# Kernel optimization log

Measured on AMD Instinct MI355X. Metric: run time of the kernel, lower is better.

The kernel has to match this reference:

```python
import jax, jax.numpy as jnp
import numpy as np

N_HEAD = 16
N_FEAT = 1024
D_K = N_FEAT // N_HEAD


def setup_inputs() -> dict:
    key = jax.random.key(0)
    ks = jax.random.split(key, 11)
    B, T1, T2 = 2, 2048, 2048
    s = 0.02
    return {
        "query": jax.random.normal(ks[0], (B, T1, N_FEAT), jnp.float32),
        "key_": jax.random.normal(ks[1], (B, T2, N_FEAT), jnp.float32),
        "value": jax.random.normal(ks[2], (B, T2, N_FEAT), jnp.float32),
        "mask": jnp.ones((B, T1, T2), jnp.int32),
        "Wq": jax.random.normal(ks[3], (N_FEAT, N_FEAT), jnp.float32) * s,
        "bq": jnp.zeros((N_FEAT,), jnp.float32),
        "Wk": jax.random.normal(ks[4], (N_FEAT, N_FEAT), jnp.float32) * s,
        "bk": jnp.zeros((N_FEAT,), jnp.float32),
        "Wv": jax.random.normal(ks[5], (N_FEAT, N_FEAT), jnp.float32) * s,
        "bv": jnp.zeros((N_FEAT,), jnp.float32),
        "Wo": jax.random.normal(ks[6], (N_FEAT, N_FEAT), jnp.float32) * s,
        "bo": jnp.zeros((N_FEAT,), jnp.float32),
    }


def reference(query, key_, value, mask, Wq, bq, Wk, bk, Wv, bv, Wo, bo):
    B = query.shape[0]
    # project and split heads: (B, T, F) -> (B, H, T, d_k)
    def heads(x, W, b):
        y = x @ W + b
        return y.reshape(B, -1, N_HEAD, D_K).transpose(0, 2, 1, 3)

    q = heads(query, Wq, bq)
    k = heads(key_, Wk, bk)
    v = heads(value, Wv, bv)

    scale = jnp.sqrt(jnp.asarray(D_K, jnp.float32))
    scores = jnp.einsum("bhqd,bhkd->bhqk", q, k) / scale  # (B,H,T1,T2)
    m = mask[:, None, :, :]  # (B,1,T1,T2)
    scores = jnp.where(m > 0, scores, jnp.asarray(-10000.0, scores.dtype))
    attn = jax.nn.softmax(scores, axis=-1)
    # dropout_rate = 0.0 / inference -> identity
    x = jnp.einsum("bhqk,bhkd->bhqd", attn, v)
    x = x.transpose(0, 2, 1, 3).reshape(B, -1, N_FEAT)
    return x @ Wo + bo
```

## Files before the change

kernel.cpp:

```cpp
#include <hip/hip_runtime.h>
#include <hip/hip_bf16.h>
#include <stdint.h>

typedef float  f32x4 __attribute__((ext_vector_type(4)));
typedef short  s16x8 __attribute__((ext_vector_type(8)));
typedef short  s16x4 __attribute__((ext_vector_type(4)));
typedef int    i32x4 __attribute__((ext_vector_type(4)));

#define DI __device__ __forceinline__

constexpr int Bb = 2, Tt = 2048, Ff = 1024, Hh = 16, Dk = 64;
constexpr int Mm = Bb * Tt;
constexpr float LOG2E = 1.44269504088896340736f;

DI ushort f2bf(float f) {
  unsigned u = __float_as_uint(f);
  unsigned r = (u + 0x7fffu + ((u >> 16) & 1u)) >> 16;
  return (ushort)r;
}

DI int cvt_pk_bf16(float lo, float hi) {
  __hip_bfloat162 t = __float22bfloat162_rn(make_float2(lo, hi));
  int w;
  __builtin_memcpy(&w, &t, 4);
  return w;
}

DI void gload16(const void* g, void* l) {
  __builtin_amdgcn_global_load_lds(
      (__attribute__((address_space(1))) void*)g,
      (__attribute__((address_space(3))) void*)l, 16, 0, 0);
}

DI void wait_vm4() { asm volatile("s_waitcnt vmcnt(4)" ::: "memory"); }
DI void wait_vm0() { asm volatile("s_waitcnt vmcnt(0)" ::: "memory"); }

__global__ __launch_bounds__(256) void prep_kernel(
    const float* __restrict__ s0, const float* __restrict__ s1, const float* __restrict__ s2,
    ushort* __restrict__ d0, ushort* __restrict__ d1, ushort* __restrict__ d2,
    const float* __restrict__ W0, const float* __restrict__ W1,
    const float* __restrict__ W2, const float* __restrict__ W3,
    ushort* __restrict__ Wt0, ushort* __restrict__ Wt1,
    ushort* __restrict__ Wt2, ushort* __restrict__ Wt3,
    const int* __restrict__ mask, int* __restrict__ flags) {
  const int bid = blockIdx.x;
  const int t = threadIdx.x;
  if (bid < 6144) {
    const int z = bid >> 11, x = bid & 2047;
    const float* src = z == 0 ? s0 : (z == 1 ? s1 : s2);
    ushort* dst = z == 0 ? d0 : (z == 1 ? d1 : d2);
    const int i = x * 256 + t;
    const float4* s4 = (const float4*)src + (size_t)i * 2;
    float4 a = s4[0], b = s4[1];
    s16x8 o;
    o[0] = (short)f2bf(a.x); o[1] = (short)f2bf(a.y); o[2] = (short)f2bf(a.z); o[3] = (short)f2bf(a.w);
    o[4] = (short)f2bf(b.x); o[5] = (short)f2bf(b.y); o[6] = (short)f2bf(b.z); o[7] = (short)f2bf(b.w);
    *((s16x8*)dst + i) = o;
  } else if (bid < 7168) {
    const int wb = bid - 6144;
    const int z = wb >> 8, bx = wb & 15, by = (wb >> 4) & 15;
    const float* W; ushort* Wt;
    switch (z) {
      case 0: W = W0; Wt = Wt0; break;
      case 1: W = W1; Wt = Wt1; break;
      case 2: W = W2; Wt = Wt2; break;
      default: W = W3; Wt = Wt3; break;
    }
    __shared__ float tile[64][65];
    const int k0 = by * 64, n0 = bx * 64;
    const int r = t >> 4, c4 = (t & 15) * 4;
#pragma unroll
    for (int i = 0; i < 4; i++) {
      const int row = r + i * 16;
      const float4 v = *(const float4*)(W + (size_t)(k0 + row) * Ff + n0 + c4);
      tile[row][c4] = v.x; tile[row][c4 + 1] = v.y; tile[row][c4 + 2] = v.z; tile[row][c4 + 3] = v.w;
    }
    __syncthreads();
#pragma unroll
    for (int i = 0; i < 4; i++) {
      const int n = r + i * 16;
      s16x4 o;
#pragma unroll
      for (int j = 0; j < 4; j++) o[j] = (short)f2bf(tile[c4 + j][n]);
      *(s16x4*)(Wt + (size_t)(n0 + n) * Ff + k0 + c4) = o;
    }
  } else {
    const int mb = bid - 7168;
    const int kb = mb & 31, qb = (mb >> 5) & 31, bz = mb >> 10;
    __shared__ int s;
    if (t == 0) s = 1;
    __syncthreads();
    int ok = 1;
#pragma unroll
    for (int i = 0; i < 4; i++) {
      const int row = qb * 64 + (t >> 4) + i * 16;
      const int4 v = *(const int4*)(mask + ((size_t)bz * Tt + row) * Tt + kb * 64 + (t & 15) * 4);
      ok &= (v.x > 0) & (v.y > 0) & (v.z > 0) & (v.w > 0);
    }
    atomicAnd(&s, ok);
    __syncthreads();
    if (t == 0) flags[(bz * 32 + qb) * 32 + kb] = s;
  }
}

DI void gemm_core(const ushort* __restrict__ A, const ushort* __restrict__ Bt,
                  const float* __restrict__ bias, void* __restrict__ Cout, float scale, int mode,
                  int m0, int n0) {
  __shared__ ushort Ads[3][128 * 32];
  __shared__ ushort Bds[3][128 * 32];
  const int tid = threadIdx.x, lane = tid & 63, w = tid >> 6;
  const int wr = w >> 1, wc = w & 1;
  const int g = lane >> 4, ln = lane & 15;
  const int strow = tid >> 2;
  const int stc = (tid & 3) * 8;

  const ushort* Asrc0 = A + (size_t)(m0 + strow) * Ff + stc;
  const ushort* Asrc1 = A + (size_t)(m0 + 64 + strow) * Ff + stc;
  const ushort* Bsrc0 = Bt + (size_t)(n0 + strow) * Ff + stc;
  const ushort* Bsrc1 = Bt + (size_t)(n0 + 64 + strow) * Ff + stc;
  const int dst0 = strow * 32 + stc;
  const int dst1 = (64 + strow) * 32 + stc;

  f32x4 acc[4][4];
#pragma unroll
  for (int m = 0; m < 4; m++)
#pragma unroll
    for (int n = 0; n < 4; n++) acc[m][n] = (f32x4){0.f, 0.f, 0.f, 0.f};

  auto stage = [&](int t, int slot) {
    const int k0 = t * 32;
    gload16(Asrc0 + k0, Ads[slot] + dst0);
    gload16(Asrc1 + k0, Ads[slot] + dst1);
    gload16(Bsrc0 + k0, Bds[slot] + dst0);
    gload16(Bsrc1 + k0, Bds[slot] + dst1);
  };

  stage(0, 0);
  stage(1, 1);

  int rs = 0, ws = 2;
  for (int t = 0; t < 32; ++t) {
    if (t < 31) wait_vm4(); else wait_vm0();
    __builtin_amdgcn_s_barrier();
    __builtin_amdgcn_sched_barrier(0);
    if (t < 30) stage(t + 2, ws);
    const ushort* As = Ads[rs];
    const ushort* Bs = Bds[rs];
    s16x8 af[4], bf[4];
#pragma unroll
    for (int m = 0; m < 4; m++) af[m] = *(const s16x8*)(As + (wr * 64 + m * 16 + ln) * 32 + g * 8);
#pragma unroll
    for (int n = 0; n < 4; n++) bf[n] = *(const s16x8*)(Bs + (wc * 64 + n * 16 + ln) * 32 + g * 8);
    __builtin_amdgcn_s_setprio(1);
#pragma unroll
    for (int m = 0; m < 4; m++)
#pragma unroll
      for (int n = 0; n < 4; n++)
        acc[m][n] = __builtin_amdgcn_mfma_f32_16x16x32_bf16(af[m], bf[n], acc[m][n], 0, 0, 0);
    __builtin_amdgcn_s_setprio(0);
    rs = rs == 2 ? 0 : rs + 1;
    ws = ws == 2 ? 0 : ws + 1;
  }
#pragma unroll
  for (int m = 0; m < 4; m++) {
    const int r0 = m0 + wr * 64 + m * 16 + g * 4;
#pragma unroll
    for (int n = 0; n < 4; n++) {
      const int col = n0 + wc * 64 + n * 16 + ln;
      const float bv = bias[col];
      if (mode == 2) {
        const int bb = r0 >> 11, rb = r0 & 2047;
        const int x = rb & 63;
        const int pbase = (x & 0x20) | ((x & 0x0C) << 1) | ((x & 0x10) >> 2);
        s16x4 o4;
#pragma unroll
        for (int r = 0; r < 4; r++) o4[r] = (short)f2bf(acc[m][n][r] + bv);
        *(s16x4*)((ushort*)Cout + ((size_t)bb * Ff + col) * Tt + (rb & ~63) + pbase) = o4;
      } else {
#pragma unroll
        for (int r = 0; r < 4; r++) {
          const float val = (acc[m][n][r] + bv) * scale;
          if (mode == 1)
            ((ushort*)Cout)[(size_t)(r0 + r) * Ff + col] = f2bf(val);
          else
            ((float*)Cout)[(size_t)(r0 + r) * Ff + col] = val;
        }
      }
    }
  }
}

__global__ __launch_bounds__(256) void qkv_gemm_kernel(
    const ushort* __restrict__ Xq, const ushort* __restrict__ Xk, const ushort* __restrict__ Xv,
    const ushort* __restrict__ Wqt, const ushort* __restrict__ Wkt, const ushort* __restrict__ Wvt,
    const float* __restrict__ bq, const float* __restrict__ bk, const float* __restrict__ bv,
    ushort* __restrict__ Qb, ushort* __restrict__ Kb, ushort* __restrict__ Vpt) {
  const int lin = blockIdx.x + 8 * blockIdx.y + 256 * blockIdx.z;
  const int work = (lin & 7) * 96 + (lin >> 3);
  const int z = work >> 8;
  const int r = work & 255;
  const int m0 = (r >> 3) * 128, n0 = (r & 7) * 128;
  const ushort* A = z == 0 ? Xq : (z == 1 ? Xk : Xv);
  const ushort* Wt = z == 0 ? Wqt : (z == 1 ? Wkt : Wvt);
  const float* bias = z == 0 ? bq : (z == 1 ? bk : bv);
  void* C = z == 0 ? (void*)Qb : (z == 1 ? (void*)Kb : (void*)Vpt);
  const float scale = z == 0 ? 0.125f * LOG2E : 1.0f;
  gemm_core(A, Wt, bias, C, scale, z == 2 ? 2 : 1, m0, n0);
}

__global__ __launch_bounds__(256) void out_gemm_kernel(const ushort* __restrict__ AO,
                                                       const ushort* __restrict__ Wot,
                                                       const float* __restrict__ bo,
                                                       float* __restrict__ Out) {
  const int lin = blockIdx.x + 8 * blockIdx.y;
  const int work = (lin & 7) * 32 + (lin >> 3);
  const int m0 = (work >> 3) * 128, n0 = (work & 7) * 128;
  gemm_core(AO, Wot, bo, Out, 1.0f, 0, m0, n0);
}

__global__ __launch_bounds__(256) void flash_kernel(
    const ushort* __restrict__ Qb, const ushort* __restrict__ Kb, const ushort* __restrict__ Vpt,
    const int* __restrict__ flags, const int* __restrict__ mask, ushort* __restrict__ AO) {
  __shared__ ushort Ks[4][64 * 64];
  __shared__ ushort Vs[4][64 * 64];
  const int lin = blockIdx.x + 16 * (blockIdx.y + 16 * blockIdx.z);
  const int work = (lin & 7) * 64 + (lin >> 3);
  const int qb = work & 15, h = (work >> 4) & 15, b = work >> 8;
  const int tid = threadIdx.x, lane = tid & 63, w = tid >> 6;
  const int g = lane >> 4, ln = lane & 15;

  const ushort* Qg = Qb + ((size_t)b * Tt + qb * 128) * Ff + h * Dk;
  const ushort* Kg = Kb + ((size_t)b * Tt) * Ff + h * Dk;
  const ushort* Vg = Vpt + (size_t)(b * Ff + h * Dk) * Tt;

  const int srow = lane >> 3;
  const int swzch = ((lane & 7) ^ srow) * 8;

  const ushort* ksrc0 = Kg + (size_t)(w * 16 + srow) * Ff + swzch;
  const ushort* ksrc1 = ksrc0 + (size_t)8 * Ff;
  const ushort* vsrc0 = Vg + (size_t)(w * 16 + srow) * Tt + swzch;
  const ushort* vsrc1 = vsrc0 + (size_t)8 * Tt;

  s16x8 qf0[2], qf1[2];
  {
    const ushort* Qrow0 = Qg + (size_t)(w * 16 + ln) * Ff;
    const ushort* Qrow1 = Qrow0 + (size_t)64 * Ff;
    qf0[0] = *(const s16x8*)(Qrow0 + g * 8);
    qf0[1] = *(const s16x8*)(Qrow0 + 32 + g * 8);
    qf1[0] = *(const s16x8*)(Qrow1 + g * 8);
    qf1[1] = *(const s16x8*)(Qrow1 + 32 + g * 8);
  }
  const int* flagrow0 = flags + (b * 32 + qb * 2) * 32;
  const int f0 = (lane < 32) ? flagrow0[lane] : 1;
  const int f1 = (lane < 32) ? flagrow0[32 + lane] : 1;

  auto stage2 = [&](ushort* Kd0, ushort* Vd0, ushort* Kd1, ushort* Vd1) {
    const int r0 = w * 16;
    gload16(ksrc0, Kd0 + r0 * 64);
    gload16(ksrc1, Kd0 + (r0 + 8) * 64);
    gload16(vsrc0, Vd0 + r0 * 64);
    gload16(vsrc1, Vd0 + (r0 + 8) * 64);
    gload16(ksrc0 + (size_t)64 * Ff, Kd1 + r0 * 64);
    gload16(ksrc1 + (size_t)64 * Ff, Kd1 + (r0 + 8) * 64);
    gload16(vsrc0 + 64, Vd1 + r0 * 64);
    gload16(vsrc1 + 64, Vd1 + (r0 + 8) * 64);
    ksrc0 += (size_t)128 * Ff; ksrc1 += (size_t)128 * Ff;
    vsrc0 += 128; vsrc1 += 128;
  };

  stage2(Ks[0], Vs[0], Ks[1], Vs[1]);
  stage2(Ks[2], Vs[2], Ks[3], Vs[3]);
  __syncthreads();
  const unsigned long long bm0 = __ballot(f0 == 0);
  const unsigned long long bm1 = __ballot(f1 == 0);

  int loff[4][2];
#pragma unroll
  for (int i = 0; i < 4; i++)
#pragma unroll
    for (int c = 0; c < 2; c++) {
      const int row = i * 16 + ln;
      loff[i][c] = row * 128 + ((c * 64 + g * 16) ^ ((row & 7) << 4));
    }
  const char* Kbase = (const char*)&Ks[0][0];
  const char* Vbase = (const char*)&Vs[0][0];

  s16x8 onesf;
#pragma unroll
  for (int j = 0; j < 8; ++j) onesf[j] = (short)0x3F80;

  f32x4 accl0 = (f32x4){0.f, 0.f, 0.f, 0.f}, accl1 = (f32x4){0.f, 0.f, 0.f, 0.f};
  f32x4 o0[4], o1[4];
#pragma unroll
  for (int ds = 0; ds < 4; ds++) { o0[ds] = (f32x4){0.f, 0.f, 0.f, 0.f}; o1[ds] = (f32x4){0.f, 0.f, 0.f, 0.f}; }

  auto body = [&](int slot, int kt) {
    const char* Kc = Kbase + slot * 8192;
    const char* Vc = Vbase + slot * 8192;
    f32x4 sf0[4], sf1[4];
    __builtin_amdgcn_s_setprio(1);
#pragma unroll
    for (int ks = 0; ks < 4; ++ks) {
      f32x4 a0 = (f32x4){0.f, 0.f, 0.f, 0.f};
      f32x4 a1 = (f32x4){0.f, 0.f, 0.f, 0.f};
#pragma unroll
      for (int c = 0; c < 2; c++) {
        const s16x8 kf = *(const s16x8*)(Kc + loff[ks][c]);
        a0 = __builtin_amdgcn_mfma_f32_16x16x32_bf16(kf, qf0[c], a0, 0, 0, 0);
        a1 = __builtin_amdgcn_mfma_f32_16x16x32_bf16(kf, qf1[c], a1, 0, 0, 0);
      }
      sf0[ks] = a0; sf1[ks] = a1;
    }
    __builtin_amdgcn_s_setprio(0);
    if ((bm0 >> kt) & 1ull) {
      const int qg_ = qb * 128 + w * 16 + ln;
#pragma unroll
      for (int ks = 0; ks < 4; ++ks) {
        const int4 mv = *(const int4*)(mask + ((size_t)b * Tt + qg_) * Tt + kt * 64 + ks * 16 + g * 4);
        if (mv.x <= 0) sf0[ks][0] = -10000.f;
        if (mv.y <= 0) sf0[ks][1] = -10000.f;
        if (mv.z <= 0) sf0[ks][2] = -10000.f;
        if (mv.w <= 0) sf0[ks][3] = -10000.f;
      }
    }
    if ((bm1 >> kt) & 1ull) {
      const int qg_ = qb * 128 + 64 + w * 16 + ln;
#pragma unroll
      for (int ks = 0; ks < 4; ++ks) {
        const int4 mv = *(const int4*)(mask + ((size_t)b * Tt + qg_) * Tt + kt * 64 + ks * 16 + g * 4);
        if (mv.x <= 0) sf1[ks][0] = -10000.f;
        if (mv.y <= 0) sf1[ks][1] = -10000.f;
        if (mv.z <= 0) sf1[ks][2] = -10000.f;
        if (mv.w <= 0) sf1[ks][3] = -10000.f;
      }
    }
#pragma unroll
    for (int ks = 0; ks < 4; ++ks) {
#pragma unroll
      for (int r = 0; r < 4; ++r) {
        sf0[ks][r] = __builtin_amdgcn_exp2f(sf0[ks][r]);
        sf1[ks][r] = __builtin_amdgcn_exp2f(sf1[ks][r]);
      }
    }
    i32x4 paw0[2], paw1[2];
#pragma unroll
    for (int c = 0; c < 2; c++)
#pragma unroll
      for (int f = 0; f < 2; f++)
#pragma unroll
        for (int hh = 0; hh < 2; hh++) {
          paw0[c][f * 2 + hh] = cvt_pk_bf16(sf0[2 * c + f][2 * hh], sf0[2 * c + f][2 * hh + 1]);
          paw1[c][f * 2 + hh] = cvt_pk_bf16(sf1[2 * c + f][2 * hh], sf1[2 * c + f][2 * hh + 1]);
        }
    const s16x8 pa00 = __builtin_bit_cast(s16x8, paw0[0]);
    const s16x8 pa01 = __builtin_bit_cast(s16x8, paw0[1]);
    const s16x8 pa10 = __builtin_bit_cast(s16x8, paw1[0]);
    const s16x8 pa11 = __builtin_bit_cast(s16x8, paw1[1]);
    __builtin_amdgcn_s_setprio(1);
    accl0 = __builtin_amdgcn_mfma_f32_16x16x32_bf16(pa00, onesf, accl0, 0, 0, 0);
    accl0 = __builtin_amdgcn_mfma_f32_16x16x32_bf16(pa01, onesf, accl0, 0, 0, 0);
    accl1 = __builtin_amdgcn_mfma_f32_16x16x32_bf16(pa10, onesf, accl1, 0, 0, 0);
    accl1 = __builtin_amdgcn_mfma_f32_16x16x32_bf16(pa11, onesf, accl1, 0, 0, 0);
#pragma unroll
    for (int ds = 0; ds < 4; ++ds) {
#pragma unroll
      for (int c = 0; c < 2; ++c) {
        const s16x8 vf = *(const s16x8*)(Vc + loff[ds][c]);
        o0[ds] = __builtin_amdgcn_mfma_f32_16x16x32_bf16(c == 0 ? pa00 : pa01, vf, o0[ds], 0, 0, 0);
        o1[ds] = __builtin_amdgcn_mfma_f32_16x16x32_bf16(c == 0 ? pa10 : pa11, vf, o1[ds], 0, 0, 0);
      }
    }
    __builtin_amdgcn_s_setprio(0);
  };

  for (int kt = 0; kt < 32; kt += 4) {
    body(0, kt);
    body(1, kt + 1);
    __syncthreads();
    if (kt + 4 < 32) stage2(Ks[0], Vs[0], Ks[1], Vs[1]);
    body(2, kt + 2);
    body(3, kt + 3);
    __syncthreads();
    if (kt + 6 < 32) stage2(Ks[2], Vs[2], Ks[3], Vs[3]);
  }

  float inv0[4], inv1[4];
#pragma unroll
  for (int r = 0; r < 4; ++r) {
    inv0[r] = 1.0f / accl0[r];
    inv1[r] = 1.0f / accl1[r];
  }
  ushort* AOg0 = AO + ((size_t)b * Tt + qb * 128 + w * 16) * Ff + h * Dk;
  ushort* AOg1 = AOg0 + (size_t)64 * Ff;
#pragma unroll
  for (int ds = 0; ds < 4; ++ds)
#pragma unroll
    for (int r = 0; r < 4; ++r) {
      AOg0[(size_t)(g * 4 + r) * Ff + ds * 16 + ln] = f2bf(o0[ds][r] * inv0[r]);
      AOg1[(size_t)(g * 4 + r) * Ff + ds * 16 + ln] = f2bf(o1[ds][r] * inv1[r]);
    }
}

extern "C" void kernel_launch(void* const* d_in, const int* in_sizes, int n_in,
                              void* d_out, int out_size, void* d_ws, size_t ws_size,
                              hipStream_t stream) {
  const float* query = (const float*)d_in[0];
  const float* key_  = (const float*)d_in[1];
  const float* value = (const float*)d_in[2];
  const int*   mask  = (const int*)d_in[3];
  const float* Wq = (const float*)d_in[4];  const float* bq = (const float*)d_in[5];
  const float* Wk = (const float*)d_in[6];  const float* bk = (const float*)d_in[7];
  const float* Wv = (const float*)d_in[8];  const float* bv = (const float*)d_in[9];
  const float* Wo = (const float*)d_in[10]; const float* bo = (const float*)d_in[11];
  float* Out = (float*)d_out;

  constexpr size_t SZ_X = (size_t)Mm * Ff * 2;
  constexpr size_t SZ_W = (size_t)Ff * Ff * 2;
  uintptr_t p = (uintptr_t)d_ws;
  auto alloc = [&](size_t sz) { void* r = (void*)p; p += (sz + 255) & ~(size_t)255; return r; };
  ushort* Xq = (ushort*)alloc(SZ_X);
  ushort* Xk = (ushort*)alloc(SZ_X);
  ushort* Xv = (ushort*)alloc(SZ_X);
  ushort* Wqt = (ushort*)alloc(SZ_W);
  ushort* Wkt = (ushort*)alloc(SZ_W);
  ushort* Wvt = (ushort*)alloc(SZ_W);
  ushort* Wot = (ushort*)alloc(SZ_W);
  ushort* Qp  = (ushort*)alloc(SZ_X);
  ushort* Kp  = (ushort*)alloc(SZ_X);
  ushort* Vpt = (ushort*)alloc(SZ_X);
  int* flags = (int*)alloc((size_t)Bb * 32 * 32 * 4);
  ushort* AO = Xq;

  prep_kernel<<<dim3(9216), 256, 0, stream>>>(query, key_, value, Xq, Xk, Xv,
                                              Wq, Wk, Wv, Wo, Wqt, Wkt, Wvt, Wot,
                                              mask, flags);
  qkv_gemm_kernel<<<dim3(8, 32, 3), 256, 0, stream>>>(Xq, Xk, Xv, Wqt, Wkt, Wvt, bq, bk, bv, Qp, Kp, Vpt);
  flash_kernel<<<dim3(16, 16, 2), 256, 0, stream>>>(Qp, Kp, Vpt, flags, mask, AO);
  out_gemm_kernel<<<dim3(8, 32), 256, 0, stream>>>(AO, Wot, bo, Out);
}
```

Measured before the change: 132.6 us.

## Software-pipeline QK of next tile with softmax/PV of current tile

Restructures the attention main loop so the QK^T MFMAs for tile k+1 are issued before the mask/exp/PV work of tile k, using two ping-pong score register sets. K/V staging changes from paired double-buffer loads to single-tile loads into a 4-slot ring, with a barrier after every tile and one tile prefetched three steps ahead. The aim is to overlap MFMA work with the exp/convert VALU work and to smooth global-to-LDS loads. In exchange it adds more register pressure from the extra score arrays, twice as many barriers, and drops the setprio hints around the QK MFMAs.

Result: slower. 150.3 us (+13.3%).

```diff
diff --git a/kernel.cpp b/kernel.cpp
--- a/kernel.cpp
+++ b/kernel.cpp
@@ -254,22 +254,19 @@
   const int f0 = (lane < 32) ? flagrow0[lane] : 1;
   const int f1 = (lane < 32) ? flagrow0[32 + lane] : 1;
 
-  auto stage2 = [&](ushort* Kd0, ushort* Vd0, ushort* Kd1, ushort* Vd1) {
+  auto stage1 = [&](ushort* Kd, ushort* Vd) {
     const int r0 = w * 16;
-    gload16(ksrc0, Kd0 + r0 * 64);
-    gload16(ksrc1, Kd0 + (r0 + 8) * 64);
-    gload16(vsrc0, Vd0 + r0 * 64);
-    gload16(vsrc1, Vd0 + (r0 + 8) * 64);
-    gload16(ksrc0 + (size_t)64 * Ff, Kd1 + r0 * 64);
-    gload16(ksrc1 + (size_t)64 * Ff, Kd1 + (r0 + 8) * 64);
-    gload16(vsrc0 + 64, Vd1 + r0 * 64);
-    gload16(vsrc1 + 64, Vd1 + (r0 + 8) * 64);
-    ksrc0 += (size_t)128 * Ff; ksrc1 += (size_t)128 * Ff;
-    vsrc0 += 128; vsrc1 += 128;
+    gload16(ksrc0, Kd + r0 * 64);
+    gload16(ksrc1, Kd + (r0 + 8) * 64);
+    gload16(vsrc0, Vd + r0 * 64);
+    gload16(vsrc1, Vd + (r0 + 8) * 64);
+    ksrc0 += (size_t)64 * Ff; ksrc1 += (size_t)64 * Ff;
+    vsrc0 += 64; vsrc1 += 64;
   };
 
-  stage2(Ks[0], Vs[0], Ks[1], Vs[1]);
-  stage2(Ks[2], Vs[2], Ks[3], Vs[3]);
+  stage1(Ks[0], Vs[0]);
+  stage1(Ks[1], Vs[1]);
+  stage1(Ks[2], Vs[2]);
   __syncthreads();
   const unsigned long long bm0 = __ballot(f0 == 0);
   const unsigned long long bm1 = __ballot(f1 == 0);
@@ -288,60 +285,57 @@
   s16x8 onesf;
 #pragma unroll
   for (int j = 0; j < 8; ++j) onesf[j] = (short)0x3F80;
-
-  f32x4 accl0 = (f32x4){0.f, 0.f, 0.f, 0.f}, accl1 = (f32x4){0.f, 0.f, 0.f, 0.f};
+  const f32x4 zz = (f32x4){0.f, 0.f, 0.f, 0.f};
+
+  f32x4 accl0 = zz, accl1 = zz;
   f32x4 o0[4], o1[4];
 #pragma unroll
-  for (int ds = 0; ds < 4; ds++) { o0[ds] = (f32x4){0.f, 0.f, 0.f, 0.f}; o1[ds] = (f32x4){0.f, 0.f, 0.f, 0.f}; }
-
-  auto body = [&](int slot, int kt) {
-    const char* Kc = Kbase + slot * 8192;
-    const char* Vc = Vbase + slot * 8192;
-    f32x4 sf0[4], sf1[4];
-    __builtin_amdgcn_s_setprio(1);
+  for (int ds = 0; ds < 4; ds++) { o0[ds] = zz; o1[ds] = zz; }
+
+  auto qk = [&](const char* Kc, f32x4 (&s0)[4], f32x4 (&s1)[4]) {
 #pragma unroll
     for (int ks = 0; ks < 4; ++ks) {
-      f32x4 a0 = (f32x4){0.f, 0.f, 0.f, 0.f};
-      f32x4 a1 = (f32x4){0.f, 0.f, 0.f, 0.f};
-#pragma unroll
-      for (int c = 0; c < 2; c++) {
-        const s16x8 kf = *(const s16x8*)(Kc + loff[ks][c]);
-        a0 = __builtin_amdgcn_mfma_f32_16x16x32_bf16(kf, qf0[c], a0, 0, 0, 0);
-        a1 = __builtin_amdgcn_mfma_f32_16x16x32_bf16(kf, qf1[c], a1, 0, 0, 0);
+      const s16x8 kfa = *(const s16x8*)(Kc + loff[ks][0]);
+      const s16x8 kfb = *(const s16x8*)(Kc + loff[ks][1]);
+      f32x4 a0 = __builtin_amdgcn_mfma_f32_16x16x32_bf16(kfa, qf0[0], zz, 0, 0, 0);
+      a0 = __builtin_amdgcn_mfma_f32_16x16x32_bf16(kfb, qf0[1], a0, 0, 0, 0);
+      f32x4 a1 = __builtin_amdgcn_mfma_f32_16x16x32_bf16(kfa, qf1[0], zz, 0, 0, 0);
+      a1 = __builtin_amdgcn_mfma_f32_16x16x32_bf16(kfb, qf1[1], a1, 0, 0, 0);
+      s0[ks] = a0; s1[ks] = a1;
+    }
+  };
+
+  auto finish = [&](int ktv, f32x4 (&s0)[4], f32x4 (&s1)[4], const char* Vc) {
+    if ((bm0 >> ktv) & 1ull) {
+      const int qg_ = qb * 128 + w * 16 + ln;
+#pragma unroll
+      for (int ks = 0; ks < 4; ++ks) {
+        const int4 mv = *(const int4*)(mask + ((size_t)b * Tt + qg_) * Tt + ktv * 64 + ks * 16 + g * 4);
+        if (mv.x <= 0) s0[ks][0] = -10000.f;
+        if (mv.y <= 0) s0[ks][1] = -10000.f;
+        if (mv.z <= 0) s0[ks][2] = -10000.f;
+        if (mv.w <= 0) s0[ks][3] = -10000.f;
       }
-      sf0[ks] = a0; sf1[ks] = a1;
-    }
-    __builtin_amdgcn_s_setprio(0);
-    if ((bm0 >> kt) & 1ull) {
-      const int qg_ = qb * 128 + w * 16 + ln;
+    }
+    if ((bm1 >> ktv) & 1ull) {
+      const int qg_ = qb * 128 + 64 + w * 16 + ln;
 #pragma unroll
       for (int ks = 0; ks < 4; ++ks) {
-        const int4 mv = *(const int4*)(mask + ((size_t)b * Tt + qg_) * Tt + kt * 64 + ks * 16 + g * 4);
-        if (mv.x <= 0) sf0[ks][0] = -10000.f;
-        if (mv.y <= 0) sf0[ks][1] = -10000.f;
-        if (mv.z <= 0) sf0[ks][2] = -10000.f;
-        if (mv.w <= 0) sf0[ks][3] = -10000.f;
+        const int4 mv = *(const int4*)(mask + ((size_t)b * Tt + qg_) * Tt + ktv * 64 + ks * 16 + g * 4);
+        if (mv.x <= 0) s1[ks][0] = -10000.f;
+        if (mv.y <= 0) s1[ks][1] = -10000.f;
+        if (mv.z <= 0) s1[ks][2] = -10000.f;
+        if (mv.w <= 0) s1[ks][3] = -10000.f;
       }
     }
-    if ((bm1 >> kt) & 1ull) {
-      const int qg_ = qb * 128 + 64 + w * 16 + ln;
-#pragma unroll
-      for (int ks = 0; ks < 4; ++ks) {
-        const int4 mv = *(const int4*)(mask + ((size_t)b * Tt + qg_) * Tt + kt * 64 + ks * 16 + g * 4);
-        if (mv.x <= 0) sf1[ks][0] = -10000.f;
-        if (mv.y <= 0) sf1[ks][1] = -10000.f;
-        if (mv.z <= 0) sf1[ks][2] = -10000.f;
-        if (mv.w <= 0) sf1[ks][3] = -10000.f;
+#pragma unroll
+    for (int ks = 0; ks < 4; ++ks) {
+#pragma unroll
+      for (int r = 0; r < 4; ++r) {
+        s0[ks][r] = __builtin_amdgcn_exp2f(s0[ks][r]);
+        s1[ks][r] = __builtin_amdgcn_exp2f(s1[ks][r]);
       }
     }
-#pragma unroll
-    for (int ks = 0; ks < 4; ++ks) {
-#pragma unroll
-      for (int r = 0; r < 4; ++r) {
-        sf0[ks][r] = __builtin_amdgcn_exp2f(sf0[ks][r]);
-        sf1[ks][r] = __builtin_amdgcn_exp2f(sf1[ks][r]);
-      }
-    }
     i32x4 paw0[2], paw1[2];
 #pragma unroll
     for (int c = 0; c < 2; c++)
@@ -349,8 +343,8 @@
       for (int f = 0; f < 2; f++)
 #pragma unroll
         for (int hh = 0; hh < 2; hh++) {
-          paw0[c][f * 2 + hh] = cvt_pk_bf16(sf0[2 * c + f][2 * hh], sf0[2 * c + f][2 * hh + 1]);
-          paw1[c][f * 2 + hh] = cvt_pk_bf16(sf1[2 * c + f][2 * hh], sf1[2 * c + f][2 * hh + 1]);
+          paw0[c][f * 2 + hh] = cvt_pk_bf16(s0[2 * c + f][2 * hh], s0[2 * c + f][2 * hh + 1]);
+          paw1[c][f * 2 + hh] = cvt_pk_bf16(s1[2 * c + f][2 * hh], s1[2 * c + f][2 * hh + 1]);
         }
     const s16x8 pa00 = __builtin_bit_cast(s16x8, paw0[0]);
     const s16x8 pa01 = __builtin_bit_cast(s16x8, paw0[1]);
@@ -373,15 +367,26 @@
     __builtin_amdgcn_s_setprio(0);
   };
 
+  f32x4 sA0[4], sA1[4], sB0[4], sB1[4];
+  qk(Kbase, sA0, sA1);
+
   for (int kt = 0; kt < 32; kt += 4) {
-    body(0, kt);
-    body(1, kt + 1);
-    __syncthreads();
-    if (kt + 4 < 32) stage2(Ks[0], Vs[0], Ks[1], Vs[1]);
-    body(2, kt + 2);
-    body(3, kt + 3);
-    __syncthreads();
-    if (kt + 6 < 32) stage2(Ks[2], Vs[2], Ks[3], Vs[3]);
+    qk(Kbase + 8192, sB0, sB1);
+    finish(kt, sA0, sA1, Vbase);
+    __syncthreads();
+    if (kt + 3 < 32) stage1(Ks[3], Vs[3]);
+    qk(Kbase + 2 * 8192, sA0, sA1);
+    finish(kt + 1, sB0, sB1, Vbase + 8192);
+    __syncthreads();
+    if (kt + 4 < 32) stage1(Ks[0], Vs[0]);
+    qk(Kbase + 3 * 8192, sB0, sB1);
+    finish(kt + 2, sA0, sA1, Vbase + 2 * 8192);
+    __syncthreads();
+    if (kt + 5 < 32) stage1(Ks[1], Vs[1]);
+    if (kt + 4 < 32) qk(Kbase, sA0, sA1);
+    finish(kt + 3, sB0, sB1, Vbase + 3 * 8192);
+    __syncthreads();
+    if (kt + 6 < 32) stage1(Ks[2], Vs[2]);
   }
 
   float inv0[4], inv1[4];
```

## Fuse fp32-to-bf16 activation conversion into QKV GEMM loads

Applied to the files above, without the earlier changes.

Removes the separate conversion pass that wrote bf16 copies of query/key/value, and instead has the QKV GEMM load fp32 activation tiles into registers, pack them to bf16, and write them to LDS with a register-staged triple-buffer pipeline. This eliminates a full read/write pass over the activations and reduces workspace. In exchange the GEMM reads twice the bytes for A tiles (repeated across column blocks) and uses more registers and VALU packing work in the main loop.

Result: faster. 124.8 us (-5.9%).

```diff
diff --git a/kernel.cpp b/kernel.cpp
--- a/kernel.cpp
+++ b/kernel.cpp
@@ -26,6 +26,13 @@
   return w;
 }
 
+DI s16x8 pack8(const float4& a, const float4& b) {
+  i32x4 w;
+  w[0] = cvt_pk_bf16(a.x, a.y); w[1] = cvt_pk_bf16(a.z, a.w);
+  w[2] = cvt_pk_bf16(b.x, b.y); w[3] = cvt_pk_bf16(b.z, b.w);
+  return __builtin_bit_cast(s16x8, w);
+}
+
 DI void gload16(const void* g, void* l) {
   __builtin_amdgcn_global_load_lds(
       (__attribute__((address_space(1))) void*)g,
@@ -33,11 +40,11 @@
 }
 
 DI void wait_vm4() { asm volatile("s_waitcnt vmcnt(4)" ::: "memory"); }
+DI void wait_vm6() { asm volatile("s_waitcnt vmcnt(6)" ::: "memory"); }
 DI void wait_vm0() { asm volatile("s_waitcnt vmcnt(0)" ::: "memory"); }
+DI void wait_lgkm0() { asm volatile("s_waitcnt lgkmcnt(0)" ::: "memory"); }
 
 __global__ __launch_bounds__(256) void prep_kernel(
-    const float* __restrict__ s0, const float* __restrict__ s1, const float* __restrict__ s2,
-    ushort* __restrict__ d0, ushort* __restrict__ d1, ushort* __restrict__ d2,
     const float* __restrict__ W0, const float* __restrict__ W1,
     const float* __restrict__ W2, const float* __restrict__ W3,
     ushort* __restrict__ Wt0, ushort* __restrict__ Wt1,
@@ -45,20 +52,8 @@
     const int* __restrict__ mask, int* __restrict__ flags) {
   const int bid = blockIdx.x;
   const int t = threadIdx.x;
-  if (bid < 6144) {
-    const int z = bid >> 11, x = bid & 2047;
-    const float* src = z == 0 ? s0 : (z == 1 ? s1 : s2);
-    ushort* dst = z == 0 ? d0 : (z == 1 ? d1 : d2);
-    const int i = x * 256 + t;
-    const float4* s4 = (const float4*)src + (size_t)i * 2;
-    float4 a = s4[0], b = s4[1];
-    s16x8 o;
-    o[0] = (short)f2bf(a.x); o[1] = (short)f2bf(a.y); o[2] = (short)f2bf(a.z); o[3] = (short)f2bf(a.w);
-    o[4] = (short)f2bf(b.x); o[5] = (short)f2bf(b.y); o[6] = (short)f2bf(b.z); o[7] = (short)f2bf(b.w);
-    *((s16x8*)dst + i) = o;
-  } else if (bid < 7168) {
-    const int wb = bid - 6144;
-    const int z = wb >> 8, bx = wb & 15, by = (wb >> 4) & 15;
+  if (bid < 1024) {
+    const int z = bid >> 8, bx = bid & 15, by = (bid >> 4) & 15;
     const float* W; ushort* Wt;
     switch (z) {
       case 0: W = W0; Wt = Wt0; break;
@@ -85,7 +80,7 @@
       *(s16x4*)(Wt + (size_t)(n0 + n) * Ff + k0 + c4) = o;
     }
   } else {
-    const int mb = bid - 7168;
+    const int mb = bid - 1024;
     const int kb = mb & 31, qb = (mb >> 5) & 31, bz = mb >> 10;
     __shared__ int s;
     if (t == 0) s = 1;
@@ -168,6 +163,98 @@
     for (int n = 0; n < 4; n++) {
       const int col = n0 + wc * 64 + n * 16 + ln;
       const float bv = bias[col];
+#pragma unroll
+      for (int r = 0; r < 4; r++) {
+        const float val = (acc[m][n][r] + bv) * scale;
+        if (mode == 1)
+          ((ushort*)Cout)[(size_t)(r0 + r) * Ff + col] = f2bf(val);
+        else
+          ((float*)Cout)[(size_t)(r0 + r) * Ff + col] = val;
+      }
+    }
+  }
+}
+
+DI void gemm_core_f32a(const float* __restrict__ A, const ushort* __restrict__ Bt,
+                       const float* __restrict__ bias, void* __restrict__ Cout, float scale,
+                       int mode, int m0, int n0) {
+  __shared__ ushort Ads[3][128 * 32];
+  __shared__ ushort Bds[3][128 * 32];
+  const int tid = threadIdx.x, lane = tid & 63, w = tid >> 6;
+  const int wr = w >> 1, wc = w & 1;
+  const int g = lane >> 4, ln = lane & 15;
+  const int strow = tid >> 2;
+  const int stc = (tid & 3) * 8;
+
+  const float*  Asrc0 = A + (size_t)(m0 + strow) * Ff + stc;
+  const float*  Asrc1 = A + (size_t)(m0 + 64 + strow) * Ff + stc;
+  const ushort* Bsrc0 = Bt + (size_t)(n0 + strow) * Ff + stc;
+  const ushort* Bsrc1 = Bt + (size_t)(n0 + 64 + strow) * Ff + stc;
+  const int dst0 = strow * 32 + stc;
+  const int dst1 = (64 + strow) * 32 + stc;
+
+  float4 rA0a, rA0b, rA1a, rA1b;
+  auto loadA = [&](int t) {
+    const float* p0 = Asrc0 + t * 32;
+    const float* p1 = Asrc1 + t * 32;
+    rA0a = *(const float4*)p0; rA0b = *(const float4*)(p0 + 4);
+    rA1a = *(const float4*)p1; rA1b = *(const float4*)(p1 + 4);
+  };
+  auto writeA = [&](int slot) {
+    *(s16x8*)(Ads[slot] + dst0) = pack8(rA0a, rA0b);
+    *(s16x8*)(Ads[slot] + dst1) = pack8(rA1a, rA1b);
+  };
+  auto stageB = [&](int t, int slot) {
+    const int k0 = t * 32;
+    gload16(Bsrc0 + k0, Bds[slot] + dst0);
+    gload16(Bsrc1 + k0, Bds[slot] + dst1);
+  };
+
+  f32x4 acc[4][4];
+#pragma unroll
+  for (int m = 0; m < 4; m++)
+#pragma unroll
+    for (int n = 0; n < 4; n++) acc[m][n] = (f32x4){0.f, 0.f, 0.f, 0.f};
+
+  loadA(0);
+  writeA(0);
+  stageB(0, 0);
+  loadA(1);
+  stageB(1, 1);
+
+  int rs = 0, ps = 1, ws = 2;
+  for (int t = 0; t < 32; ++t) {
+    if (t < 31) wait_vm6(); else wait_vm0();
+    wait_lgkm0();
+    __builtin_amdgcn_s_barrier();
+    __builtin_amdgcn_sched_barrier(0);
+    if (t < 31) writeA(ps);
+    if (t < 30) { loadA(t + 2); stageB(t + 2, ws); }
+    const ushort* As = Ads[rs];
+    const ushort* Bs = Bds[rs];
+    s16x8 af[4], bf[4];
+#pragma unroll
+    for (int m = 0; m < 4; m++) af[m] = *(const s16x8*)(As + (wr * 64 + m * 16 + ln) * 32 + g * 8);
+#pragma unroll
+    for (int n = 0; n < 4; n++) bf[n] = *(const s16x8*)(Bs + (wc * 64 + n * 16 + ln) * 32 + g * 8);
+    __builtin_amdgcn_s_setprio(1);
+#pragma unroll
+    for (int m = 0; m < 4; m++)
+#pragma unroll
+      for (int n = 0; n < 4; n++)
+        acc[m][n] = __builtin_amdgcn_mfma_f32_16x16x32_bf16(af[m], bf[n], acc[m][n], 0, 0, 0);
+    __builtin_amdgcn_s_setprio(0);
+    rs = rs == 2 ? 0 : rs + 1;
+    ps = ps == 2 ? 0 : ps + 1;
+    ws = ws == 2 ? 0 : ws + 1;
+  }
+#pragma unroll
+  for (int m = 0; m < 4; m++) {
+    const int r0 = m0 + wr * 64 + m * 16 + g * 4;
+#pragma unroll
+    for (int n = 0; n < 4; n++) {
+      const int col = n0 + wc * 64 + n * 16 + ln;
+      const float bv = bias[col];
       if (mode == 2) {
         const int bb = r0 >> 11, rb = r0 & 2047;
         const int x = rb & 63;
@@ -178,20 +265,15 @@
         *(s16x4*)((ushort*)Cout + ((size_t)bb * Ff + col) * Tt + (rb & ~63) + pbase) = o4;
       } else {
 #pragma unroll
-        for (int r = 0; r < 4; r++) {
-          const float val = (acc[m][n][r] + bv) * scale;
-          if (mode == 1)
-            ((ushort*)Cout)[(size_t)(r0 + r) * Ff + col] = f2bf(val);
-          else
-            ((float*)Cout)[(size_t)(r0 + r) * Ff + col] = val;
-        }
+        for (int r = 0; r < 4; r++)
+          ((ushort*)Cout)[(size_t)(r0 + r) * Ff + col] = f2bf((acc[m][n][r] + bv) * scale);
       }
     }
   }
 }
 
 __global__ __launch_bounds__(256) void qkv_gemm_kernel(
-    const ushort* __restrict__ Xq, const ushort* __restrict__ Xk, const ushort* __restrict__ Xv,
+    const float* __restrict__ Xq, const float* __restrict__ Xk, const float* __restrict__ Xv,
     const ushort* __restrict__ Wqt, const ushort* __restrict__ Wkt, const ushort* __restrict__ Wvt,
     const float* __restrict__ bq, const float* __restrict__ bk, const float* __restrict__ bv,
     ushort* __restrict__ Qb, ushort* __restrict__ Kb, ushort* __restrict__ Vpt) {
@@ -200,12 +282,12 @@
   const int z = work >> 8;
   const int r = work & 255;
   const int m0 = (r >> 3) * 128, n0 = (r & 7) * 128;
-  const ushort* A = z == 0 ? Xq : (z == 1 ? Xk : Xv);
+  const float* A = z == 0 ? Xq : (z == 1 ? Xk : Xv);
   const ushort* Wt = z == 0 ? Wqt : (z == 1 ? Wkt : Wvt);
   const float* bias = z == 0 ? bq : (z == 1 ? bk : bv);
   void* C = z == 0 ? (void*)Qb : (z == 1 ? (void*)Kb : (void*)Vpt);
   const float scale = z == 0 ? 0.125f * LOG2E : 1.0f;
-  gemm_core(A, Wt, bias, C, scale, z == 2 ? 2 : 1, m0, n0);
+  gemm_core_f32a(A, Wt, bias, C, scale, z == 2 ? 2 : 1, m0, n0);
 }
 
 __global__ __launch_bounds__(256) void out_gemm_kernel(const ushort* __restrict__ AO,
@@ -418,9 +500,7 @@
   constexpr size_t SZ_W = (size_t)Ff * Ff * 2;
   uintptr_t p = (uintptr_t)d_ws;
   auto alloc = [&](size_t sz) { void* r = (void*)p; p += (sz + 255) & ~(size_t)255; return r; };
-  ushort* Xq = (ushort*)alloc(SZ_X);
-  ushort* Xk = (ushort*)alloc(SZ_X);
-  ushort* Xv = (ushort*)alloc(SZ_X);
+  ushort* AO  = (ushort*)alloc(SZ_X);
   ushort* Wqt = (ushort*)alloc(SZ_W);
   ushort* Wkt = (ushort*)alloc(SZ_W);
   ushort* Wvt = (ushort*)alloc(SZ_W);
@@ -429,12 +509,10 @@
   ushort* Kp  = (ushort*)alloc(SZ_X);
   ushort* Vpt = (ushort*)alloc(SZ_X);
   int* flags = (int*)alloc((size_t)Bb * 32 * 32 * 4);
-  ushort* AO = Xq;
-
-  prep_kernel<<<dim3(9216), 256, 0, stream>>>(query, key_, value, Xq, Xk, Xv,
-                                              Wq, Wk, Wv, Wo, Wqt, Wkt, Wvt, Wot,
-                                              mask, flags);
-  qkv_gemm_kernel<<<dim3(8, 32, 3), 256, 0, stream>>>(Xq, Xk, Xv, Wqt, Wkt, Wvt, bq, bk, bv, Qp, Kp, Vpt);
+
+  prep_kernel<<<dim3(3072), 256, 0, stream>>>(Wq, Wk, Wv, Wo, Wqt, Wkt, Wvt, Wot, mask, flags);
+  qkv_gemm_kernel<<<dim3(8, 32, 3), 256, 0, stream>>>(query, key_, value, Wqt, Wkt, Wvt,
+                                                      bq, bk, bv, Qp, Kp, Vpt);
   flash_kernel<<<dim3(16, 16, 2), 256, 0, stream>>>(Qp, Kp, Vpt, flags, mask, AO);
   out_gemm_kernel<<<dim3(8, 32), 256, 0, stream>>>(AO, Wot, bo, Out);
 }
```
